# Kernel optimization log

Measured on AMD Instinct MI355X. Metric: run time of the kernel, lower is better.

## Reference

```python
import jax, jax.numpy as jnp
import numpy as np

NUM_STEPS = 151
STEP = 2.0 / (NUM_STEPS - 1)
TSIZE = NUM_STEPS  # t = -1, -1+step, ..., 1
N = 4096
D = 512
NUM_CLASSES = 100


def setup_inputs() -> dict:
    key = jax.random.key(0)
    k1, k2 = jax.random.split(key)
    feats = jax.random.normal(k1, (N, D), dtype=jnp.float32)
    # L2-normalize so pairwise dot products lie in [-1, 1] (histogram support)
    feats = feats / jnp.linalg.norm(feats, axis=1, keepdims=True)
    classes = jax.random.randint(k2, (N,), 0, NUM_CLASSES, dtype=jnp.int64)
    return {"features": feats, "classes": classes}


def reference(features, classes):
    n = features.shape[0]
    # pairwise cosine similarities, upper triangle (i < j)
    dists = features @ features.T  # [N, N]
    iu, ju = jnp.triu_indices(n, k=1)  # static index arrays
    s = dists[iu, ju]                  # [P] similarities
    pos = classes[iu] == classes[ju]   # [P] same-class mask

    # triangular soft-binning exactly as in the torch code:
    # f = floor(s/step)*step; bin at t==f gets (s-f)/step, bin at t==f+step gets (f+step-s)/step
    f = jnp.floor(s / STEP) * STEP
    j = jnp.floor(s / STEP).astype(jnp.int32) + (NUM_STEPS - 1) // 2  # index of t == f
    wa = (s - f) / STEP
    wb = (f + STEP - s) / STEP
    va = (j >= 0) & (j < TSIZE)
    vb = (j + 1 >= 0) & (j + 1 < TSIZE)
    ja = jnp.clip(j, 0, TSIZE - 1)
    jb = jnp.clip(j + 1, 0, TSIZE - 1)

    def hist(mask, size):
        w_a = jnp.where(va & mask, wa, 0.0)
        w_b = jnp.where(vb & mask, wb, 0.0)
        h = jnp.zeros(TSIZE, s.dtype).at[ja].add(w_a).at[jb].add(w_b)
        return h / size.astype(s.dtype)

    pos_size = pos.sum()
    neg_size = (~pos).sum()
    hist_pos = hist(pos, pos_size)
    hist_neg = hist(~pos, neg_size)
    # tril-masked repeat + sum(0) == inclusive cumulative sum of hist_pos
    hist_pos_cdf = jnp.cumsum(hist_pos)
    loss = jnp.sum(hist_neg * hist_pos_cdf)
    return loss
```

## Files before the change

### kernel.cpp

```cpp
#include <hip/hip_runtime.h>


#define N_PTS   4096
#define DIM     512
#define TSIZE   151
#define HALF_T  75
#define BM      128
#define BK      64
#define NSTEP   24
#define NPAIR   528
#define P_TOTAL 8386560u
#define STEPF   (2.0f / 150.0f)
#define STEPINV 75.0f
#define NCOPY   8
#define HSTRIDE 309
#define GRID    576
#define NROWS   (2 * TSIZE + 1)

typedef short bfrag __attribute__((ext_vector_type(8)));
typedef float ffrag __attribute__((ext_vector_type(4)));
typedef unsigned short u16;
typedef unsigned int   u32;

__device__ __forceinline__ ffrag mfma16(bfrag a, bfrag b, ffrag c) {
  return __builtin_amdgcn_mfma_f32_16x16x32_bf16(a, b, c, 0, 0, 0);
}

__device__ __forceinline__ void split4(float4 v, uint2* hi, uint2* lo) {
  u32 u0 = __float_as_uint(v.x), u1 = __float_as_uint(v.y);
  u32 u2 = __float_as_uint(v.z), u3 = __float_as_uint(v.w);
  float r0 = v.x - __uint_as_float(u0 & 0xFFFF0000u);
  float r1 = v.y - __uint_as_float(u1 & 0xFFFF0000u);
  float r2 = v.z - __uint_as_float(u2 & 0xFFFF0000u);
  float r3 = v.w - __uint_as_float(u3 & 0xFFFF0000u);
  hi->x = (u0 >> 16) | (u1 & 0xFFFF0000u);
  hi->y = (u2 >> 16) | (u3 & 0xFFFF0000u);
  lo->x = (__float_as_uint(r0) >> 16) | (__float_as_uint(r1) & 0xFFFF0000u);
  lo->y = (__float_as_uint(r2) >> 16) | (__float_as_uint(r3) & 0xFFFF0000u);
}

__device__ __forceinline__ bool tile_decode(int bid, int* bi_, int* bj_) {
  const int xcd = bid & 7, slot = bid >> 3;
  if (xcd < 6) {
    if (slot >= 64) return false;
    const int BA[6] = {0, 0, 0, 1, 1, 2};
    const int BB[6] = {1, 2, 3, 2, 3, 3};
    *bi_ = BA[xcd] * 8 + (slot >> 3);
    *bj_ = BB[xcd] * 8 + (slot & 7);
  } else {
    int p = slot;
    int band = (xcd - 6) * 2 + (p >= 36 ? 1 : 0);
    if (p >= 36) p -= 36;
    int rem = p, cnt = 8, ii = 0;
    while (rem >= cnt) { rem -= cnt; --cnt; ++ii; }
    *bi_ = band * 8 + ii;
    *bj_ = band * 8 + ii + rem;
  }
  return true;
}

__device__ __forceinline__ int pair_index(int bi, int bj) {
  return bi * 32 - bi * (bi - 1) / 2 + (bj - bi);
}

__device__ __forceinline__ void stage_step(
    int s, u16* Ad, u16* Bd,
    const u16* __restrict__ Fhi, const u16* __restrict__ Flo,
    int rowA, int rowB, int w, int rseg, int swzk)
{
  const int region = s >> 3;
  const int k0 = (s & 7) * BK;
  const u16* ap = (region == 1) ? Flo : Fhi;
  const u16* bp = (region == 2) ? Flo : Fhi;
  #pragma unroll
  for (int g = 0; g < 4; ++g) {
    int seg = w * 4 + g;
    int row = seg * 8 + rseg;
    size_t ga = (size_t)(rowA + row) * DIM + k0 + swzk;
    size_t gb = (size_t)(rowB + row) * DIM + k0 + swzk;
    __builtin_amdgcn_global_load_lds(
        (const __attribute__((address_space(1))) unsigned int*)(ap + ga),
        (__attribute__((address_space(3))) unsigned int*)(Ad + seg * 512),
        16, 0, 0);
    __builtin_amdgcn_global_load_lds(
        (const __attribute__((address_space(1))) unsigned int*)(bp + gb),
        (__attribute__((address_space(3))) unsigned int*)(Bd + seg * 512),
        16, 0, 0);
  }
}

__device__ __forceinline__ void compute_step(
    const u16* As, const u16* Bs, ffrag (&acc)[4][4],
    int wy, int wx, int l4, int l16)
{
  const int swz = (l16 & 7) << 3;
  #pragma unroll
  for (int ks = 0; ks < 2; ++ks) {
    bfrag a[4], b[4];
    #pragma unroll
    for (int f = 0; f < 4; ++f) {
      int ra = wy * 64 + f * 16 + l16;
      int rb = wx * 64 + f * 16 + l16;
      int ko = (ks * 32 + l4 * 8) ^ swz;
      a[f] = *(const bfrag*)(As + ra * BK + ko);
      b[f] = *(const bfrag*)(Bs + rb * BK + ko);
    }
    #pragma unroll
    for (int fj = 0; fj < 4; ++fj)
      #pragma unroll
      for (int fi = 0; fi < 4; ++fi)
        acc[fi][fj] = mfma16(a[fi], b[fj], acc[fi][fj]);
  }
}

__device__ __forceinline__ void bin_epilogue(
    const ffrag (&acc)[4][4], float* h, const int* clsA, const int* clsB,
    int wy, int wx, int l4, int l16, bool diag, u32* myPos)
{
  #pragma unroll
  for (int fi = 0; fi < 4; ++fi) {
    #pragma unroll
    for (int fj = 0; fj < 4; ++fj) {
      #pragma unroll
      for (int r = 0; r < 4; ++r) {
        int li = wy * 64 + fi * 16 + l4 * 4 + r;
        int lj = wx * 64 + fj * 16 + l16;
        if (diag && li >= lj) continue;
        float s  = acc[fi][fj][r];
        float jf = floorf(s * STEPINV);
        int   jb = (int)jf + HALF_T;
        float f  = jf * STEPF;
        float wa = (s - f) * STEPINV;
        float wb = (f + STEPF - s) * STEPINV;
        bool  pos = (clsA[li] == clsB[lj]);
        *myPos += pos ? 1u : 0u;
        int off = pos ? 0 : TSIZE;
        if (jb >= 0 && jb < TSIZE)         unsafeAtomicAdd(h + off + jb, wa);
        if (jb + 1 >= 0 && jb + 1 < TSIZE) unsafeAtomicAdd(h + off + jb + 1, wb);
      }
    }
  }
}

__global__ __launch_bounds__(256) void presplit(
    const float* __restrict__ F, u16* __restrict__ Fhi, u16* __restrict__ Flo,
    float* __restrict__ g_hist)
{
  int u = blockIdx.x * 256 + threadIdx.x;
  int row = u >> 6, kb = u & 63;
  const float* src = F + (size_t)row * DIM + kb * 8;
  float4 v0 = *(const float4*)(src);
  float4 v1 = *(const float4*)(src + 4);
  uint2 h0, l0, h1, l1;
  split4(v0, &h0, &l0);
  split4(v1, &h1, &l1);
  uint4 hv; hv.x = h0.x; hv.y = h0.y; hv.z = h1.x; hv.w = h1.y;
  uint4 lv; lv.x = l0.x; lv.y = l0.y; lv.z = l1.x; lv.w = l1.y;
  size_t dst = (size_t)row * DIM + kb * 8;
  *(uint4*)(Fhi + dst) = hv;
  *(uint4*)(Flo + dst) = lv;
  if (blockIdx.x == 0) {
    for (int i = threadIdx.x; i < NROWS; i += 256) g_hist[i] = 0.0f;
  }
}

template <int PART>
__global__ __launch_bounds__(256, 3) void hist_mfma(
    const u16* __restrict__ Fhi, const u16* __restrict__ Flo,
    const int* __restrict__ cls,
    float* __restrict__ g_hist, float* __restrict__ partial)
{
  __shared__ __align__(16) u16 As[BM * BK];
  __shared__ __align__(16) u16 Bs[BM * BK];
  __shared__ float hist[NCOPY * HSTRIDE];
  __shared__ int clsA[BM], clsB[BM];
  __shared__ u32 posCount;

  int bi, bj;
  if (!tile_decode((int)blockIdx.x, &bi, &bj)) return;
  const int t = threadIdx.x;
  const int rowA = bi * BM, rowB = bj * BM;

  for (int i = t; i < NCOPY * HSTRIDE; i += 256) hist[i] = 0.0f;
  if (t < BM) clsA[t] = cls[rowA + t];
  else        clsB[t - BM] = cls[rowB + (t - BM)];
  if (t == 0) posCount = 0u;

  const int lane = t & 63, w = t >> 6;
  const int wy = w >> 1, wx = w & 1;
  const int l4 = lane >> 4, l16 = lane & 15;
  const int rseg = lane >> 3;
  const int swzk = ((lane & 7) ^ (lane >> 3)) << 3;

  ffrag acc[4][4] = {};

  #pragma unroll 1
  for (int s = 0; s < NSTEP; ++s) {
    __syncthreads();
    stage_step(s, As, Bs, Fhi, Flo, rowA, rowB, w, rseg, swzk);
    __syncthreads();
    compute_step(As, Bs, acc, wy, wx, l4, l16);
  }

  u32 myPos = 0;
  float* h = hist + (lane & 7) * HSTRIDE;
  bin_epilogue(acc, h, clsA, clsB, wy, wx, l4, l16, bi == bj, &myPos);
  atomicAdd(&posCount, myPos);
  __syncthreads();

  if (PART) {
    const int p = pair_index(bi, bj);
    for (int i = t; i < 2 * TSIZE; i += 256) {
      float v = 0.0f;
      #pragma unroll
      for (int c = 0; c < NCOPY; ++c) v += hist[c * HSTRIDE + i];
      partial[(size_t)i * NPAIR + p] = v;
    }
    if (t == 0) partial[(size_t)(2 * TSIZE) * NPAIR + p] = (float)posCount;
  } else {
    for (int i = t; i < 2 * TSIZE; i += 256) {
      float v = 0.0f;
      #pragma unroll
      for (int c = 0; c < NCOPY; ++c) v += hist[c * HSTRIDE + i];
      unsafeAtomicAdd(g_hist + i, v);
    }
    if (t == 0) unsafeAtomicAdd(g_hist + 2 * TSIZE, (float)posCount);
  }
}

__global__ __launch_bounds__(256) void reduce_partials(
    const float* __restrict__ partial, float* __restrict__ g_hist)
{
  const int wv = blockIdx.x * 4 + (threadIdx.x >> 6);
  const int lane = threadIdx.x & 63;
  if (wv >= NROWS) return;
  float s = 0.0f;
  for (int p = lane; p < NPAIR; p += 64) s += partial[(size_t)wv * NPAIR + p];
  #pragma unroll
  for (int o = 32; o > 0; o >>= 1) s += __shfl_down(s, o);
  if (lane == 0) g_hist[wv] = s;
}

__global__ __launch_bounds__(256) void finalize(
    const float* __restrict__ g_hist, float* __restrict__ out)
{
  __shared__ float hp[TSIZE];
  __shared__ float hn[TSIZE];
  __shared__ float red[4];
  const int t = threadIdx.x;
  const float Np = g_hist[2 * TSIZE];
  const float Nn = (float)P_TOTAL - Np;
  if (t < TSIZE) {
    hp[t] = g_hist[t] / Np;
    hn[t] = g_hist[TSIZE + t] / Nn;
  }
  __syncthreads();
  for (int off = 1; off < TSIZE; off <<= 1) {
    float v = 0.0f;
    if (t < TSIZE && t >= off) v = hp[t - off];
    __syncthreads();
    if (t < TSIZE) hp[t] += v;
    __syncthreads();
  }
  float term = (t < TSIZE) ? hn[t] * hp[t] : 0.0f;
  #pragma unroll
  for (int o = 32; o > 0; o >>= 1) term += __shfl_down(term, o);
  if ((t & 63) == 0) red[t >> 6] = term;
  __syncthreads();
  if (t == 0) *out = red[0] + red[1] + red[2] + red[3];
}

extern "C" void kernel_launch(void* const* d_in, const int* in_sizes, int n_in,
                              void* d_out, int out_size, void* d_ws, size_t ws_size,
                              hipStream_t stream) {
  const float* F   = (const float*)d_in[0];
  const int*   cls = (const int*)d_in[1];
  float* g_hist = (float*)d_ws;
  float* out = (float*)d_out;

  const size_t offH   = 65536;
  const size_t bytesP = (size_t)N_PTS * DIM * sizeof(u16);
  const size_t offPar = offH + 2 * bytesP;
  const size_t bytesPar = (size_t)NROWS * NPAIR * sizeof(float);
  u16* Fhi = (u16*)((char*)d_ws + offH);
  u16* Flo = (u16*)((char*)d_ws + offH + bytesP);

  presplit<<<(N_PTS * 64) / 256, 256, 0, stream>>>(F, Fhi, Flo, g_hist);
  if (ws_size >= offPar + bytesPar) {
    float* partial = (float*)((char*)d_ws + offPar);
    hist_mfma<1><<<GRID, 256, 0, stream>>>(Fhi, Flo, cls, g_hist, partial);
    reduce_partials<<<(NROWS + 3) / 4, 256, 0, stream>>>(partial, g_hist);
  } else {
    hist_mfma<0><<<GRID, 256, 0, stream>>>(Fhi, Flo, cls, g_hist, nullptr);
  }
  finalize<<<1, 256, 0, stream>>>(g_hist, out);
}
```

Before: 224.8 us.

## Triple-buffer LDS tiles with async prefetch and fuse reduce with finalize

The MFMA histogram kernel now keeps three LDS buffers per operand and issues global loads for step s+1 before computing step s. It uses a vmcnt wait and a single barrier per step instead of two __syncthreads. The aim is to hide global load latency behind MFMA work. The partial-sum reduction and finalize are merged into one 1024-thread kernel, and the atomic fallback path is removed, cutting a launch. The triple buffer roughly triples tile LDS use and drops the occupancy hint of 3 blocks. It also assumes the workspace is large enough for partials.

```diff
diff --git a/kernel.cpp b/kernel.cpp
--- a/kernel.cpp
+++ b/kernel.cpp
@@ -8,6 +8,7 @@
 #define BM      128
 #define BK      64
 #define NSTEP   24
+#define NBUF    3
 #define NPAIR   528
 #define P_TOTAL 8386560u
 #define STEPF   (2.0f / 150.0f)
@@ -143,8 +144,7 @@
 }
 
 __global__ __launch_bounds__(256) void presplit(
-    const float* __restrict__ F, u16* __restrict__ Fhi, u16* __restrict__ Flo,
-    float* __restrict__ g_hist)
+    const float* __restrict__ F, u16* __restrict__ Fhi, u16* __restrict__ Flo)
 {
   int u = blockIdx.x * 256 + threadIdx.x;
   int row = u >> 6, kb = u & 63;
@@ -159,19 +159,14 @@
   size_t dst = (size_t)row * DIM + kb * 8;
   *(uint4*)(Fhi + dst) = hv;
   *(uint4*)(Flo + dst) = lv;
-  if (blockIdx.x == 0) {
-    for (int i = threadIdx.x; i < NROWS; i += 256) g_hist[i] = 0.0f;
-  }
-}
-
-template <int PART>
-__global__ __launch_bounds__(256, 3) void hist_mfma(
+}
+
+__global__ __launch_bounds__(256) void hist_mfma(
     const u16* __restrict__ Fhi, const u16* __restrict__ Flo,
-    const int* __restrict__ cls,
-    float* __restrict__ g_hist, float* __restrict__ partial)
-{
-  __shared__ __align__(16) u16 As[BM * BK];
-  __shared__ __align__(16) u16 Bs[BM * BK];
+    const int* __restrict__ cls, float* __restrict__ partial)
+{
+  __shared__ __align__(16) u16 AS[NBUF][BM * BK];
+  __shared__ __align__(16) u16 BS[NBUF][BM * BK];
   __shared__ float hist[NCOPY * HSTRIDE];
   __shared__ int clsA[BM], clsB[BM];
   __shared__ u32 posCount;
@@ -194,12 +189,19 @@
 
   ffrag acc[4][4] = {};
 
+  stage_step(0, AS[0], BS[0], Fhi, Flo, rowA, rowB, w, rseg, swzk);
+
   #pragma unroll 1
   for (int s = 0; s < NSTEP; ++s) {
-    __syncthreads();
-    stage_step(s, As, Bs, Fhi, Flo, rowA, rowB, w, rseg, swzk);
-    __syncthreads();
-    compute_step(As, Bs, acc, wy, wx, l4, l16);
+    if (s + 1 < NSTEP) {
+      stage_step(s + 1, AS[(s + 1) % NBUF], BS[(s + 1) % NBUF],
+                 Fhi, Flo, rowA, rowB, w, rseg, swzk);
+      asm volatile("s_waitcnt vmcnt(8)" ::: "memory");
+    } else {
+      asm volatile("s_waitcnt vmcnt(0)" ::: "memory");
+    }
+    __builtin_amdgcn_s_barrier();
+    compute_step(AS[s % NBUF], BS[s % NBUF], acc, wy, wx, l4, l16);
   }
 
   u32 myPos = 0;
@@ -208,51 +210,39 @@
   atomicAdd(&posCount, myPos);
   __syncthreads();
 
-  if (PART) {
-    const int p = pair_index(bi, bj);
-    for (int i = t; i < 2 * TSIZE; i += 256) {
-      float v = 0.0f;
-      #pragma unroll
-      for (int c = 0; c < NCOPY; ++c) v += hist[c * HSTRIDE + i];
-      partial[(size_t)i * NPAIR + p] = v;
-    }
-    if (t == 0) partial[(size_t)(2 * TSIZE) * NPAIR + p] = (float)posCount;
-  } else {
-    for (int i = t; i < 2 * TSIZE; i += 256) {
-      float v = 0.0f;
-      #pragma unroll
-      for (int c = 0; c < NCOPY; ++c) v += hist[c * HSTRIDE + i];
-      unsafeAtomicAdd(g_hist + i, v);
-    }
-    if (t == 0) unsafeAtomicAdd(g_hist + 2 * TSIZE, (float)posCount);
-  }
-}
-
-__global__ __launch_bounds__(256) void reduce_partials(
-    const float* __restrict__ partial, float* __restrict__ g_hist)
-{
-  const int wv = blockIdx.x * 4 + (threadIdx.x >> 6);
-  const int lane = threadIdx.x & 63;
-  if (wv >= NROWS) return;
-  float s = 0.0f;
-  for (int p = lane; p < NPAIR; p += 64) s += partial[(size_t)wv * NPAIR + p];
-  #pragma unroll
-  for (int o = 32; o > 0; o >>= 1) s += __shfl_down(s, o);
-  if (lane == 0) g_hist[wv] = s;
-}
-
-__global__ __launch_bounds__(256) void finalize(
-    const float* __restrict__ g_hist, float* __restrict__ out)
-{
+  const int p = pair_index(bi, bj);
+  for (int i = t; i < 2 * TSIZE; i += 256) {
+    float v = 0.0f;
+    #pragma unroll
+    for (int c = 0; c < NCOPY; ++c) v += hist[c * HSTRIDE + i];
+    partial[(size_t)i * NPAIR + p] = v;
+  }
+  if (t == 0) partial[(size_t)(2 * TSIZE) * NPAIR + p] = (float)posCount;
+}
+
+__global__ __launch_bounds__(1024) void reduce_finalize(
+    const float* __restrict__ partial, float* __restrict__ out)
+{
+  __shared__ float hsum[NROWS];
   __shared__ float hp[TSIZE];
   __shared__ float hn[TSIZE];
-  __shared__ float red[4];
-  const int t = threadIdx.x;
-  const float Np = g_hist[2 * TSIZE];
+  __shared__ float red[16];
+  const int t = threadIdx.x, wv = t >> 6, lane = t & 63;
+
+  for (int r = wv; r < NROWS; r += 16) {
+    float s = 0.0f;
+    for (int p = lane; p < NPAIR; p += 64) s += partial[(size_t)r * NPAIR + p];
+    #pragma unroll
+    for (int o = 32; o > 0; o >>= 1) s += __shfl_down(s, o);
+    if (lane == 0) hsum[r] = s;
+  }
+  __syncthreads();
+
+  const float Np = hsum[2 * TSIZE];
   const float Nn = (float)P_TOTAL - Np;
   if (t < TSIZE) {
-    hp[t] = g_hist[t] / Np;
-    hn[t] = g_hist[TSIZE + t] / Nn;
+    hp[t] = hsum[t] / Np;
+    hn[t] = hsum[TSIZE + t] / Nn;
   }
   __syncthreads();
   for (int off = 1; off < TSIZE; off <<= 1) {
@@ -267,7 +257,12 @@
   for (int o = 32; o > 0; o >>= 1) term += __shfl_down(term, o);
   if ((t & 63) == 0) red[t >> 6] = term;
   __syncthreads();
-  if (t == 0) *out = red[0] + red[1] + red[2] + red[3];
+  if (t == 0) {
+    float s = 0.0f;
+    #pragma unroll
+    for (int i = 0; i < 16; ++i) s += red[i];
+    *out = s;
+  }
 }
 
 extern "C" void kernel_launch(void* const* d_in, const int* in_sizes, int n_in,
@@ -275,23 +270,16 @@
                               hipStream_t stream) {
   const float* F   = (const float*)d_in[0];
   const int*   cls = (const int*)d_in[1];
-  float* g_hist = (float*)d_ws;
   float* out = (float*)d_out;
 
   const size_t offH   = 65536;
   const size_t bytesP = (size_t)N_PTS * DIM * sizeof(u16);
   const size_t offPar = offH + 2 * bytesP;
-  const size_t bytesPar = (size_t)NROWS * NPAIR * sizeof(float);
   u16* Fhi = (u16*)((char*)d_ws + offH);
   u16* Flo = (u16*)((char*)d_ws + offH + bytesP);
-
-  presplit<<<(N_PTS * 64) / 256, 256, 0, stream>>>(F, Fhi, Flo, g_hist);
-  if (ws_size >= offPar + bytesPar) {
-    float* partial = (float*)((char*)d_ws + offPar);
-    hist_mfma<1><<<GRID, 256, 0, stream>>>(Fhi, Flo, cls, g_hist, partial);
-    reduce_partials<<<(NROWS + 3) / 4, 256, 0, stream>>>(partial, g_hist);
-  } else {
-    hist_mfma<0><<<GRID, 256, 0, stream>>>(Fhi, Flo, cls, g_hist, nullptr);
-  }
-  finalize<<<1, 256, 0, stream>>>(g_hist, out);
-}
+  float* partial = (float*)((char*)d_ws + offPar);
+
+  presplit<<<(N_PTS * 64) / 256, 256, 0, stream>>>(F, Fhi, Flo);
+  hist_mfma<<<GRID, 256, 0, stream>>>(Fhi, Flo, cls, partial);
+  reduce_finalize<<<1, 1024, 0, stream>>>(partial, out);
+}
```

New measurement: 293.4 us. +30.5%, slower.
